# Kernel tuning notes

Hardware: AMD Instinct MI355X
Metric: run time of the kernel (lower is better)

## Reference

```python
import jax, jax.numpy as jnp
import numpy as np

N_MESH = 128
BOX_SIZE = 12.8
SPACING = BOX_SIZE / N_MESH  # 0.1
N_POINTS = 100000
N_CHANNELS = 16


def setup_inputs() -> dict:
    key = jax.random.key(0)
    k1, k2 = jax.random.split(key)
    mesh_values = jax.random.normal(k1, (N_CHANNELS, N_MESH, N_MESH, N_MESH), dtype=jnp.float32)
    points = jax.random.uniform(k2, (N_POINTS, 3), dtype=jnp.float32) * BOX_SIZE
    return {"mesh_values": mesh_values, "points": points}


def reference(mesh_values, points):
    # points in real space -> fractional grid coordinates
    pc = points / SPACING                       # [N, 3]
    rp = jnp.round(pc).astype(jnp.int32)        # nearest grid point [N, 3]
    dist = pc - rp.astype(pc.dtype)             # [N, 3], in [-0.5, 0.5]
    # quadratic (order-3) interpolation weights for offsets -1, 0, +1
    w_m = (2.0 * dist - 1.0) ** 2 / 8.0
    w_0 = 0.75 - dist * dist
    w_p = (2.0 * dist + 1.0) ** 2 / 8.0
    w = jnp.stack([w_m, w_0, w_p], axis=0)      # [3, N, 3] (offset, point, axis)
    # periodic-wrapped indices for offsets -1, 0, +1
    idx = (rp[None, :, :] + jnp.array([-1, 0, 1], dtype=jnp.int32)[:, None, None]) % N_MESH  # [3, N, 3]
    # all 27 offset combinations
    ox, oy, oz = jnp.meshgrid(jnp.arange(3), jnp.arange(3), jnp.arange(3), indexing="ij")
    ox, oy, oz = ox.ravel(), oy.ravel(), oz.ravel()  # [27]
    ix = idx[ox, :, 0]  # [27, N]
    iy = idx[oy, :, 1]
    iz = idx[oz, :, 2]
    lin = (ix * N_MESH + iy) * N_MESH + iz      # [27, N] linear mesh index
    gathered = mesh_values.reshape(N_CHANNELS, -1)[:, lin]   # [C, 27, N]
    weight = w[ox, :, 0] * w[oy, :, 1] * w[oz, :, 2]          # [27, N]
    out = jnp.einsum("con,on->nc", gathered, weight)          # [N, C]
    return out
```

## Files before the change

kernel.cpp:

```cpp
#include <hip/hip_runtime.h>
#include <hip/hip_fp16.h>

#define NMESH 128
#define NMESH2 (128 * 128)
#define NMESH3 (128 * 128 * 128)
#define NPOINTS 100000
#define NCH 16

#define NBINS_DIM 16
#define NBINS 4096
#define BINW 8
#define HALO 10
#define BIN_CAP 64

__global__ __launch_bounds__(256) void transpose_to_half_v4(
    const float* __restrict__ in,
    __half* __restrict__ outT)
{
    __shared__ float lds[2][NCH * 256];
    const int t = threadIdx.x;
    const int f = t & 63;
    const int c0 = t >> 6;
    const int nTiles = NMESH3 / 256;

    int buf = 0;
    for (int tile = blockIdx.x; tile < nTiles; tile += gridDim.x, buf ^= 1) {
        const int s_base = tile * 256;
#pragma unroll
        for (int k = 0; k < 4; ++k) {
            const int c = (c0 + 4 * k + tile) & 15;
            const float4 v =
                *(const float4*)(in + (size_t)c * NMESH3 + s_base + 4 * f);
            *(float4*)&lds[buf][c * 256 + 4 * f] = v;
        }
        __syncthreads();
        uint4* o = (uint4*)(outT + (size_t)s_base * NCH);
#pragma unroll
        for (int r = 0; r < 2; ++r) {
            const int i = t + 256 * r;
            const int s = i >> 1;
            const int h = (i & 1) * 8;
            uint32_t w[4];
#pragma unroll
            for (int m = 0; m < 4; ++m) {
                const float f0 = lds[buf][(h + 2 * m + 0) * 256 + s];
                const float f1 = lds[buf][(h + 2 * m + 1) * 256 + s];
                w[m] = (uint32_t)__half_as_ushort(__float2half(f0)) |
                       ((uint32_t)__half_as_ushort(__float2half(f1)) << 16);
            }
            o[i] = make_uint4(w[0], w[1], w[2], w[3]);
        }
    }
}

__global__ __launch_bounds__(256) void bin_zero_kernel(int* __restrict__ bin_count)
{
    const int i = blockIdx.x * 256 + threadIdx.x;
    if (i < NBINS) bin_count[i] = 0;
}

__global__ __launch_bounds__(256) void bin_scatter_kernel(
    const float* __restrict__ pts,
    int* __restrict__ bin_count,
    int* __restrict__ sorted_p)
{
    const int p = blockIdx.x * 256 + threadIdx.x;
    if (p >= NPOINTS) return;

    const float SP = 0.1f;
    const float pcx = pts[p * 3 + 0] / SP;
    const float pcy = pts[p * 3 + 1] / SP;
    const float pcz = pts[p * 3 + 2] / SP;
    const int rxw = (int)rintf(pcx) & (NMESH - 1);
    const int ryw = (int)rintf(pcy) & (NMESH - 1);
    const int rzw = (int)rintf(pcz) & (NMESH - 1);

    const int b = ((rxw >> 3) << 8) | ((ryw >> 3) << 4) | (rzw >> 3);
    const int slot = atomicAdd(&bin_count[b], 1);
    if (slot < BIN_CAP) sorted_p[b * BIN_CAP + slot] = p;
}

__global__ __launch_bounds__(256) void binned_gather_kernel(
    const __half* __restrict__ meshT,
    const float* __restrict__ pts,
    const int* __restrict__ bin_count,
    const int* __restrict__ sorted_p,
    float4* __restrict__ out)
{
    __shared__ __half tile[HALO * HALO * HALO * NCH];

    const int b = blockIdx.x;
    const int bx = b >> 8;
    const int by = (b >> 4) & 15;
    const int bz = b & 15;
    const int gx0 = bx * BINW - 1;
    const int gy0 = by * BINW - 1;
    const int gz0 = bz * BINW - 1;

    for (int ci = threadIdx.x; ci < HALO * HALO * HALO; ci += 256) {
        const int lx = ci / 100;
        const int rem = ci - lx * 100;
        const int ly = rem / 10;
        const int lz = rem - ly * 10;
        const int gx = (gx0 + lx) & (NMESH - 1);
        const int gy = (gy0 + ly) & (NMESH - 1);
        const int gz = (gz0 + lz) & (NMESH - 1);
        const uint4* src =
            (const uint4*)(meshT + ((size_t)(gx * NMESH + gy) * NMESH + gz) * NCH);
        uint4* dst = (uint4*)(tile + ci * NCH);
        dst[0] = src[0];
        dst[1] = src[1];
    }
    __syncthreads();

    const int cnt = min(bin_count[b], BIN_CAP);
    const int q = threadIdx.x & 3;

    for (int g = threadIdx.x >> 2; g < cnt; g += 64) {
        const int p = sorted_p[b * BIN_CAP + g];

        const float SP = 0.1f;
        const float pcx = pts[p * 3 + 0] / SP;
        const float pcy = pts[p * 3 + 1] / SP;
        const float pcz = pts[p * 3 + 2] / SP;

        const int rx = (int)rintf(pcx);
        const int ry = (int)rintf(pcy);
        const int rz = (int)rintf(pcz);

        const float dx = pcx - (float)rx;
        const float dy = pcy - (float)ry;
        const float dz = pcz - (float)rz;

        float wX[3], wY[3], wZ[3];
        wX[0] = (2.0f * dx - 1.0f) * (2.0f * dx - 1.0f) * 0.125f;
        wX[1] = 0.75f - dx * dx;
        wX[2] = (2.0f * dx + 1.0f) * (2.0f * dx + 1.0f) * 0.125f;
        wY[0] = (2.0f * dy - 1.0f) * (2.0f * dy - 1.0f) * 0.125f;
        wY[1] = 0.75f - dy * dy;
        wY[2] = (2.0f * dy + 1.0f) * (2.0f * dy + 1.0f) * 0.125f;
        wZ[0] = (2.0f * dz - 1.0f) * (2.0f * dz - 1.0f) * 0.125f;
        wZ[1] = 0.75f - dz * dz;
        wZ[2] = (2.0f * dz + 1.0f) * (2.0f * dz + 1.0f) * 0.125f;

        const int lrx = (rx & (NMESH - 1)) - bx * BINW + 1;
        const int lry = (ry & (NMESH - 1)) - by * BINW + 1;
        const int lrz = (rz & (NMESH - 1)) - bz * BINW + 1;

        float4 acc = make_float4(0.0f, 0.0f, 0.0f, 0.0f);
#pragma unroll
        for (int a = 0; a < 3; ++a) {
#pragma unroll
            for (int bb = 0; bb < 3; ++bb) {
                const int lx = lrx - 1 + a;
                const int ly = lry - 1 + bb;
                const __half* base =
                    tile + ((lx * HALO + ly) * HALO + (lrz - 1)) * NCH + q * 4;
                const float wxy = wX[a] * wY[bb];
#pragma unroll
                for (int k = 0; k < 3; ++k) {
                    union { uint2 u; __half2 h[2]; } d;
                    d.u = *(const uint2*)(base + k * NCH);
                    const float2 f01 = __half22float2(d.h[0]);
                    const float2 f23 = __half22float2(d.h[1]);
                    const float w = wxy * wZ[k];
                    acc.x = fmaf(f01.x, w, acc.x);
                    acc.y = fmaf(f01.y, w, acc.y);
                    acc.z = fmaf(f23.x, w, acc.z);
                    acc.w = fmaf(f23.y, w, acc.w);
                }
            }
        }
        out[p * 4 + q] = acc;
    }
}

__global__ __launch_bounds__(256) void mesh_interp_fallback_kernel(
    const float* __restrict__ mesh,
    const float* __restrict__ pts,
    float* __restrict__ out)
{
    const int tid = blockIdx.x * 256 + threadIdx.x;
    const int c = tid & (NCH - 1);
    const int p = tid >> 4;
    if (p >= NPOINTS) return;

    const float SP = 0.1f;
    const float pcx = pts[p * 3 + 0] / SP;
    const float pcy = pts[p * 3 + 1] / SP;
    const float pcz = pts[p * 3 + 2] / SP;

    const int rx = (int)rintf(pcx);
    const int ry = (int)rintf(pcy);
    const int rz = (int)rintf(pcz);

    const float dx = pcx - (float)rx;
    const float dy = pcy - (float)ry;
    const float dz = pcz - (float)rz;

    float wX[3], wY[3], wZ[3];
    wX[0] = (2.0f * dx - 1.0f) * (2.0f * dx - 1.0f) * 0.125f;
    wX[1] = 0.75f - dx * dx;
    wX[2] = (2.0f * dx + 1.0f) * (2.0f * dx + 1.0f) * 0.125f;
    wY[0] = (2.0f * dy - 1.0f) * (2.0f * dy - 1.0f) * 0.125f;
    wY[1] = 0.75f - dy * dy;
    wY[2] = (2.0f * dy + 1.0f) * (2.0f * dy + 1.0f) * 0.125f;
    wZ[0] = (2.0f * dz - 1.0f) * (2.0f * dz - 1.0f) * 0.125f;
    wZ[1] = 0.75f - dz * dz;
    wZ[2] = (2.0f * dz + 1.0f) * (2.0f * dz + 1.0f) * 0.125f;

    int xb[3], yb[3], zi[3];
#pragma unroll
    for (int k = 0; k < 3; ++k) {
        xb[k] = ((rx - 1 + k) & (NMESH - 1)) * NMESH2;
        yb[k] = ((ry - 1 + k) & (NMESH - 1)) * NMESH;
        zi[k] = ((rz - 1 + k) & (NMESH - 1));
    }

    const float* __restrict__ mc = mesh + (size_t)c * NMESH3;
    float acc = 0.0f;
#pragma unroll
    for (int a = 0; a < 3; ++a) {
#pragma unroll
        for (int b = 0; b < 3; ++b) {
            const float* __restrict__ row = mc + xb[a] + yb[b];
            const float wxy = wX[a] * wY[b];
            acc = fmaf(row[zi[0]], wxy * wZ[0], acc);
            acc = fmaf(row[zi[1]], wxy * wZ[1], acc);
            acc = fmaf(row[zi[2]], wxy * wZ[2], acc);
        }
    }
    out[tid] = acc;
}

extern "C" void kernel_launch(void* const* d_in, const int* in_sizes, int n_in,
                              void* d_out, int out_size, void* d_ws, size_t ws_size,
                              hipStream_t stream) {
    const float* mesh = (const float*)d_in[0];
    const float* pts  = (const float*)d_in[1];

    const size_t meshT_bytes = (size_t)NMESH3 * NCH * sizeof(__half);
    const size_t count_bytes = (size_t)NBINS * sizeof(int);
    const size_t sorted_bytes = (size_t)NBINS * BIN_CAP * sizeof(int);
    const size_t needed = meshT_bytes + count_bytes + sorted_bytes;

    if (ws_size >= needed) {
        __half* meshT = (__half*)d_ws;
        int* bin_count = (int*)((char*)d_ws + meshT_bytes);
        int* sorted_p = bin_count + NBINS;

        transpose_to_half_v4<<<2048, 256, 0, stream>>>(mesh, meshT);
        bin_zero_kernel<<<NBINS / 256, 256, 0, stream>>>(bin_count);
        bin_scatter_kernel<<<(NPOINTS + 255) / 256, 256, 0, stream>>>(
            pts, bin_count, sorted_p);
        binned_gather_kernel<<<NBINS, 256, 0, stream>>>(
            meshT, pts, bin_count, sorted_p, (float4*)d_out);
    } else {
        const int total = NPOINTS * NCH;
        mesh_interp_fallback_kernel<<<(total + 255) / 256, 256, 0, stream>>>(
            mesh, pts, (float*)d_out);
    }
}
```

Before: 240.8 us.

## Fuse mesh fp32-to-half transpose into binned gather tile load

Removes the separate full-mesh transpose/half-conversion kernel and has each bin block load its halo directly from the channel-major fp32 mesh. Each block converts values to half and writes them into a padded LDS tile (16-wide z extent, pitch 272) using float4 reads along z, then runs the 27-point stencil from LDS. Block size goes to 512 threads. This avoids writing and rereading a 64MB half-precision copy of the mesh, at the cost of loading a wider z halo (16 instead of 10) and doing the conversion redundantly across overlapping halos.

Result: slower. 297.6 us (+23.6%).

```diff
diff --git a/kernel.cpp b/kernel.cpp
--- a/kernel.cpp
+++ b/kernel.cpp
@@ -7,51 +7,13 @@
 #define NPOINTS 100000
 #define NCH 16
 
-#define NBINS_DIM 16
 #define NBINS 4096
 #define BINW 8
-#define HALO 10
 #define BIN_CAP 64
 
-__global__ __launch_bounds__(256) void transpose_to_half_v4(
-    const float* __restrict__ in,
-    __half* __restrict__ outT)
-{
-    __shared__ float lds[2][NCH * 256];
-    const int t = threadIdx.x;
-    const int f = t & 63;
-    const int c0 = t >> 6;
-    const int nTiles = NMESH3 / 256;
-
-    int buf = 0;
-    for (int tile = blockIdx.x; tile < nTiles; tile += gridDim.x, buf ^= 1) {
-        const int s_base = tile * 256;
-#pragma unroll
-        for (int k = 0; k < 4; ++k) {
-            const int c = (c0 + 4 * k + tile) & 15;
-            const float4 v =
-                *(const float4*)(in + (size_t)c * NMESH3 + s_base + 4 * f);
-            *(float4*)&lds[buf][c * 256 + 4 * f] = v;
-        }
-        __syncthreads();
-        uint4* o = (uint4*)(outT + (size_t)s_base * NCH);
-#pragma unroll
-        for (int r = 0; r < 2; ++r) {
-            const int i = t + 256 * r;
-            const int s = i >> 1;
-            const int h = (i & 1) * 8;
-            uint32_t w[4];
-#pragma unroll
-            for (int m = 0; m < 4; ++m) {
-                const float f0 = lds[buf][(h + 2 * m + 0) * 256 + s];
-                const float f1 = lds[buf][(h + 2 * m + 1) * 256 + s];
-                w[m] = (uint32_t)__half_as_ushort(__float2half(f0)) |
-                       ((uint32_t)__half_as_ushort(__float2half(f1)) << 16);
-            }
-            o[i] = make_uint4(w[0], w[1], w[2], w[3]);
-        }
-    }
-}
+#define HALOXY 10
+#define ZW 16
+#define PITCH_US 272
 
 __global__ __launch_bounds__(256) void bin_zero_kernel(int* __restrict__ bin_count)
 {
@@ -68,55 +30,63 @@
     if (p >= NPOINTS) return;
 
     const float SP = 0.1f;
-    const float pcx = pts[p * 3 + 0] / SP;
-    const float pcy = pts[p * 3 + 1] / SP;
-    const float pcz = pts[p * 3 + 2] / SP;
-    const int rxw = (int)rintf(pcx) & (NMESH - 1);
-    const int ryw = (int)rintf(pcy) & (NMESH - 1);
-    const int rzw = (int)rintf(pcz) & (NMESH - 1);
+    const int rxw = (int)rintf(pts[p * 3 + 0] / SP) & (NMESH - 1);
+    const int ryw = (int)rintf(pts[p * 3 + 1] / SP) & (NMESH - 1);
+    const int rzw = (int)rintf(pts[p * 3 + 2] / SP) & (NMESH - 1);
 
     const int b = ((rxw >> 3) << 8) | ((ryw >> 3) << 4) | (rzw >> 3);
     const int slot = atomicAdd(&bin_count[b], 1);
     if (slot < BIN_CAP) sorted_p[b * BIN_CAP + slot] = p;
 }
 
-__global__ __launch_bounds__(256) void binned_gather_kernel(
-    const __half* __restrict__ meshT,
+__global__ __launch_bounds__(512) void fused_binned_gather_kernel(
+    const float* __restrict__ mesh,
     const float* __restrict__ pts,
     const int* __restrict__ bin_count,
     const int* __restrict__ sorted_p,
     float4* __restrict__ out)
 {
-    __shared__ __half tile[HALO * HALO * HALO * NCH];
+    __shared__ unsigned short tile[HALOXY * HALOXY * PITCH_US];
 
     const int b = blockIdx.x;
     const int bx = b >> 8;
     const int by = (b >> 4) & 15;
     const int bz = b & 15;
-    const int gx0 = bx * BINW - 1;
-    const int gy0 = by * BINW - 1;
-    const int gz0 = bz * BINW - 1;
-
-    for (int ci = threadIdx.x; ci < HALO * HALO * HALO; ci += 256) {
-        const int lx = ci / 100;
-        const int rem = ci - lx * 100;
-        const int ly = rem / 10;
-        const int lz = rem - ly * 10;
-        const int gx = (gx0 + lx) & (NMESH - 1);
-        const int gy = (gy0 + ly) & (NMESH - 1);
-        const int gz = (gz0 + lz) & (NMESH - 1);
-        const uint4* src =
-            (const uint4*)(meshT + ((size_t)(gx * NMESH + gy) * NMESH + gz) * NCH);
-        uint4* dst = (uint4*)(tile + ci * NCH);
-        dst[0] = src[0];
-        dst[1] = src[1];
+
+    uint32_t* tile32 = (uint32_t*)tile;
+    for (int j = threadIdx.x; j < 8 * HALOXY * HALOXY * 4; j += 512) {
+        const int zc  = j & 3;
+        const int t2  = j >> 2;
+        const int ly  = t2 % 10;
+        const int t3  = t2 / 10;
+        const int lx  = t3 % 10;
+        const int cp  = t3 / 10;
+
+        const int gx = (bx * BINW - 1 + lx) & (NMESH - 1);
+        const int gy = (by * BINW - 1 + ly) & (NMESH - 1);
+        const int gz = (bz * BINW - 4 + 4 * zc) & (NMESH - 1);
+        const size_t sidx = (size_t)(gx * NMESH + gy) * NMESH + gz;
+
+        const float4 fa = *(const float4*)(mesh + (size_t)(2 * cp + 0) * NMESH3 + sidx);
+        const float4 fb = *(const float4*)(mesh + (size_t)(2 * cp + 1) * NMESH3 + sidx);
+
+        const float fav[4] = {fa.x, fa.y, fa.z, fa.w};
+        const float fbv[4] = {fb.x, fb.y, fb.z, fb.w};
+        const int row = lx * 10 + ly;
+#pragma unroll
+        for (int jz = 0; jz < 4; ++jz) {
+            const uint32_t u =
+                (uint32_t)__half_as_ushort(__float2half(fav[jz])) |
+                ((uint32_t)__half_as_ushort(__float2half(fbv[jz])) << 16);
+            tile32[row * (PITCH_US / 2) + (4 * zc + jz) * 8 + cp] = u;
+        }
     }
     __syncthreads();
 
     const int cnt = min(bin_count[b], BIN_CAP);
     const int q = threadIdx.x & 3;
 
-    for (int g = threadIdx.x >> 2; g < cnt; g += 64) {
+    for (int g = threadIdx.x >> 2; g < cnt; g += 128) {
         const int p = sorted_p[b * BIN_CAP + g];
 
         const float SP = 0.1f;
@@ -145,17 +115,16 @@
 
         const int lrx = (rx & (NMESH - 1)) - bx * BINW + 1;
         const int lry = (ry & (NMESH - 1)) - by * BINW + 1;
-        const int lrz = (rz & (NMESH - 1)) - bz * BINW + 1;
+        const int lrz = (rz & (NMESH - 1)) - bz * BINW + 4;
 
         float4 acc = make_float4(0.0f, 0.0f, 0.0f, 0.0f);
 #pragma unroll
         for (int a = 0; a < 3; ++a) {
 #pragma unroll
             for (int bb = 0; bb < 3; ++bb) {
-                const int lx = lrx - 1 + a;
-                const int ly = lry - 1 + bb;
-                const __half* base =
-                    tile + ((lx * HALO + ly) * HALO + (lrz - 1)) * NCH + q * 4;
+                const int row = (lrx - 1 + a) * 10 + (lry - 1 + bb);
+                const unsigned short* base =
+                    tile + row * PITCH_US + (lrz - 1) * NCH + q * 4;
                 const float wxy = wX[a] * wY[bb];
 #pragma unroll
                 for (int k = 0; k < 3; ++k) {
@@ -239,22 +208,19 @@
     const float* mesh = (const float*)d_in[0];
     const float* pts  = (const float*)d_in[1];
 
-    const size_t meshT_bytes = (size_t)NMESH3 * NCH * sizeof(__half);
     const size_t count_bytes = (size_t)NBINS * sizeof(int);
     const size_t sorted_bytes = (size_t)NBINS * BIN_CAP * sizeof(int);
-    const size_t needed = meshT_bytes + count_bytes + sorted_bytes;
+    const size_t needed = count_bytes + sorted_bytes;
 
     if (ws_size >= needed) {
-        __half* meshT = (__half*)d_ws;
-        int* bin_count = (int*)((char*)d_ws + meshT_bytes);
+        int* bin_count = (int*)d_ws;
         int* sorted_p = bin_count + NBINS;
 
-        transpose_to_half_v4<<<2048, 256, 0, stream>>>(mesh, meshT);
         bin_zero_kernel<<<NBINS / 256, 256, 0, stream>>>(bin_count);
         bin_scatter_kernel<<<(NPOINTS + 255) / 256, 256, 0, stream>>>(
             pts, bin_count, sorted_p);
-        binned_gather_kernel<<<NBINS, 256, 0, stream>>>(
-            meshT, pts, bin_count, sorted_p, (float4*)d_out);
+        fused_binned_gather_kernel<<<NBINS, 512, 0, stream>>>(
+            mesh, pts, bin_count, sorted_p, (float4*)d_out);
     } else {
         const int total = NPOINTS * NCH;
         mesh_interp_fallback_kernel<<<(total + 255) / 256, 256, 0, stream>>>(
```
